# Optimization experiments

Measured on AMD Instinct MI355X. Metric: run time of the kernel, lower is better.

Reference implementation:

```python
import jax, jax.numpy as jnp
import numpy as np

SHIFTS = 1
WINDOW_SIZES = (4, 8, 16)
BN_EPS = 1e-5


def _calc_attn_path(x, ws, shifts):
    # x: (b, H, W, 2c) with channels laid out as (qv=2, c)
    b, H, W, c2 = x.shape
    c = c2 // 2
    if shifts > 0:
        x = jnp.roll(x, shift=(-ws // 2, -ws // 2), axis=(1, 2))
    h, w = H // ws, W // ws
    # 'b (h dh) (w dw) (qv c) -> qv (b h w) (dh dw c)'
    qv = x.reshape(b, h, ws, w, ws, 2, c).transpose(5, 0, 1, 3, 2, 4, 6)
    qv = qv.reshape(2, b * h * w, ws * ws * c)
    q, v = qv[0], qv[1]                       # (N, D), N = b*h*w windows, D = ws*ws*c
    atn = jax.nn.softmax(q @ q.T, axis=-1)    # (N, N) attention across windows (as in source)
    y = atn @ v                               # (N, D)
    # '(b h w) (dh dw c) -> b (h dh) (w dw) c'
    y = y.reshape(b, h, w, ws, ws, c).transpose(0, 1, 3, 2, 4, 5).reshape(b, H, W, c)
    if shifts > 0:
        y = jnp.roll(y, shift=(ws // 2, ws // 2), axis=(1, 2))
    return y, atn


def setup_inputs() -> dict:
    key = jax.random.key(0)
    ks = jax.random.split(key, 3)
    B, H, W, C = 4, 128, 128, 180
    inputs = jax.random.normal(ks[0], (B, H, W, C), jnp.float32)
    conv1_w = jax.random.normal(ks[1], (1, 1, C, 2 * C), jnp.float32) * 0.05
    conv1_b = jnp.zeros((2 * C,), jnp.float32)
    bn_scale = jnp.ones((2 * C,), jnp.float32)
    bn_bias = jnp.zeros((2 * C,), jnp.float32)
    conv2_w = jax.random.normal(ks[2], (1, 1, C, C), jnp.float32) * 0.05
    conv2_b = jnp.zeros((C,), jnp.float32)
    return {"inputs": inputs, "conv1_w": conv1_w, "conv1_b": conv1_b,
            "bn_scale": bn_scale, "bn_bias": bn_bias,
            "conv2_w": conv2_w, "conv2_b": conv2_b}


def reference(inputs, conv1_w, conv1_b, bn_scale, bn_bias, conv2_w, conv2_b):
    # 1x1 conv to 2*C channels (calc_attn=True)
    x = jnp.einsum('bhwc,cd->bhwd', inputs, conv1_w[0, 0]) + conv1_b
    # BatchNorm in training mode (batch statistics)
    mean = x.mean(axis=(0, 1, 2))
    var = x.var(axis=(0, 1, 2))
    x = (x - mean) * jax.lax.rsqrt(var + BN_EPS) * bn_scale + bn_bias
    xs = jnp.split(x, 3, axis=-1)             # three groups of 2*C/3 channels
    ys, attns = [], []
    for ws, xi in zip(WINDOW_SIZES, xs):
        y, a = _calc_attn_path(xi, ws, SHIFTS)
        ys.append(y)
        attns.append(a)
    y = jnp.concatenate(ys, axis=-1)          # back to C channels
    y = jnp.einsum('bhwc,cd->bhwd', y, conv2_w[0, 0]) + conv2_b
    return (y, *attns)
```

## Files before the change

kernel.cpp:

```cpp
#include <hip/hip_runtime.h>

typedef unsigned short u16;
typedef __bf16 bf16x8 __attribute__((ext_vector_type(8)));
typedef float f32x4 __attribute__((ext_vector_type(4)));
typedef u16 u16x4 __attribute__((ext_vector_type(4)));
typedef u16 u16x8 __attribute__((ext_vector_type(8)));

__device__ __forceinline__ u16 f2bf(float v) {
    unsigned u = __float_as_uint(v);
    unsigned r = (u + 0x7fffu + ((u >> 16) & 1u)) >> 16;
    return (u16)r;
}
__device__ __forceinline__ float bf2f(u16 u) { return __uint_as_float(((unsigned)u) << 16); }

__device__ __forceinline__ void async_cp16(const u16* g, u16* l) {
    __builtin_amdgcn_global_load_lds((const __attribute__((address_space(1))) unsigned int*)g,
                                     (__attribute__((address_space(3))) unsigned int*)l, 16, 0, 0);
}

__device__ __forceinline__ int xcd_swz(int local, int n) {
    const int q = n >> 3, r = n & 7;
    const int xcd = local & 7, j = local >> 3;
    const int base = xcd < r ? xcd * (q + 1) : r * (q + 1) + (xcd - r) * q;
    return base + j;
}

#define LKSWZ(tid) ((((tid) & 3) ^ (((tid) >> 3) & 3)) << 3)
#define ROSWZ(lane) (((lane) & 15) * 32 + ((((lane) >> 4) ^ (((lane) >> 1) & 3)) << 3))

__global__ __launch_bounds__(256) void gemm_f32(
    const u16* __restrict__ A, const u16* __restrict__ B,
    float* __restrict__ C, const float* __restrict__ bias,
    int K, int ldc, int n_store)
{
    __shared__ char smem[32768];
    u16* As = (u16*)smem;
    u16* Bs = (u16*)(smem + 8192);
    const int tid = threadIdx.x;
    const int lane = tid & 63;
    const int wave = tid >> 6;
    const int wm = wave >> 1, wn = wave & 1;
    const long m0 = (long)blockIdx.y * 128;
    const long n0 = (long)blockIdx.x * 128;

    f32x4 acc[4][4] = {};
    const int lrow = tid >> 2;
    const int lk = LKSWZ(tid);
    const u16* Ag = A + (m0 + lrow) * (long)K + lk;
    const u16* Bg = B + (n0 + lrow) * (long)K + lk;
    u16* Asl = As + tid * 8;
    u16* Bsl = Bs + tid * 8;
    const long K64 = (long)64 * K;
    const int ro = ROSWZ(lane);
    const int nsteps = K >> 5;

    async_cp16(Ag, Asl);
    async_cp16(Ag + K64, Asl + 2048);
    async_cp16(Bg, Bsl);
    async_cp16(Bg + K64, Bsl + 2048);
    __syncthreads();

    int cur = 0;
    for (int s = 0; s < nsteps; s++) {
        if (s + 1 < nsteps) {
            const int kn = (s + 1) << 5;
            u16* An = Asl + ((cur ^ 1) << 13);
            u16* Bn = Bsl + ((cur ^ 1) << 13);
            async_cp16(Ag + kn, An);
            async_cp16(Ag + kn + K64, An + 2048);
            async_cp16(Bg + kn, Bn);
            async_cp16(Bg + kn + K64, Bn + 2048);
        }
        bf16x8 af[4], bg[4];
        const u16* Asc = As + (cur << 13);
        const u16* Bsc = Bs + (cur << 13);
#pragma unroll
        for (int i = 0; i < 4; i++) af[i] = *(const bf16x8*)(Asc + (wm * 64 + i * 16) * 32 + ro);
#pragma unroll
        for (int j = 0; j < 4; j++) bg[j] = *(const bf16x8*)(Bsc + (wn * 64 + j * 16) * 32 + ro);
#pragma unroll
        for (int i = 0; i < 4; i++)
#pragma unroll
            for (int j = 0; j < 4; j++)
                acc[i][j] = __builtin_amdgcn_mfma_f32_16x16x32_bf16(af[i], bg[j], acc[i][j], 0, 0, 0);
        __syncthreads();
        cur ^= 1;
    }

    float bv[4];
#pragma unroll
    for (int j = 0; j < 4; j++) bv[j] = bias[n0 + wn * 64 + j * 16 + (lane & 15)];

    float* Cs = (float*)smem;
    for (int c = 0; c < 4; c++) {
        __syncthreads();
        if (wm == (c >> 1)) {
#pragma unroll
            for (int ii = 0; ii < 2; ii++) {
                const int i = (c & 1) * 2 + ii;
#pragma unroll
                for (int j = 0; j < 4; j++)
#pragma unroll
                    for (int r = 0; r < 4; r++) {
                        const int lr = ii * 16 + ((lane >> 4) << 2) + r;
                        Cs[lr * 128 + wn * 64 + j * 16 + (lane & 15)] = acc[i][j][r] + bv[j];
                    }
            }
        }
        __syncthreads();
        const int lr = tid >> 3;
        const int cg = (tid & 7) * 16;
        const long rowg = m0 + c * 32 + lr;
#pragma unroll
        for (int e = 0; e < 4; e++) {
            const int colg = cg + e * 4;
            if ((int)n0 + colg < n_store)
                *(f32x4*)(C + rowg * (long)ldc + n0 + colg) = *(const f32x4*)(Cs + lr * 128 + colg);
        }
    }
}

__global__ __launch_bounds__(256) void conv1_gemm(
    const float* __restrict__ A, const u16* __restrict__ B,
    u16* __restrict__ C, const float* __restrict__ bias, float* __restrict__ accum)
{
    __shared__ char smem[16384];
    u16* As = (u16*)smem;
    u16* Bs = (u16*)(smem + 8192);
    const int tid = threadIdx.x;
    const int lane = tid & 63;
    const int wave = tid >> 6;
    const int wm = wave >> 1, wn = wave & 1;
    const long m0 = (long)blockIdx.y * 128;
    const long n0 = (long)blockIdx.x * 128;

    f32x4 acc[4][4] = {};
    const int lrow = tid >> 2;
    const int lk = LKSWZ(tid);
    const float* Ar0 = A + (m0 + lrow) * 180L;
    const float* Ar1 = Ar0 + 64 * 180L;
    const u16* Bg = B + (n0 + lrow) * 192L + lk;
    u16* Asl = As + tid * 8;
    u16* Bsl = Bs + tid * 8;
    const int ro = ROSWZ(lane);

#pragma unroll
    for (int k0 = 0; k0 < 192; k0 += 32) {
        const int gk = k0 + lk;
        u16x8 oa, ob;
        if (gk + 8 <= 180) {
            f32x4 a0 = *(const f32x4*)(Ar0 + gk), a1 = *(const f32x4*)(Ar0 + gk + 4);
            f32x4 b0 = *(const f32x4*)(Ar1 + gk), b1 = *(const f32x4*)(Ar1 + gk + 4);
#pragma unroll
            for (int c = 0; c < 4; c++) {
                oa[c] = f2bf(a0[c]); oa[4 + c] = f2bf(a1[c]);
                ob[c] = f2bf(b0[c]); ob[4 + c] = f2bf(b1[c]);
            }
        } else if (gk < 180) {
            f32x4 a0 = *(const f32x4*)(Ar0 + gk);
            f32x4 b0 = *(const f32x4*)(Ar1 + gk);
#pragma unroll
            for (int c = 0; c < 4; c++) {
                oa[c] = f2bf(a0[c]); oa[4 + c] = 0;
                ob[c] = f2bf(b0[c]); ob[4 + c] = 0;
            }
        } else {
#pragma unroll
            for (int c = 0; c < 8; c++) { oa[c] = 0; ob[c] = 0; }
        }
        *(u16x8*)Asl = oa;
        *(u16x8*)(Asl + 2048) = ob;
        async_cp16(Bg + k0, Bsl);
        async_cp16(Bg + k0 + 64 * 192, Bsl + 2048);
        __syncthreads();
        bf16x8 af[4], bg[4];
#pragma unroll
        for (int i = 0; i < 4; i++) af[i] = *(const bf16x8*)(As + (wm * 64 + i * 16) * 32 + ro);
#pragma unroll
        for (int j = 0; j < 4; j++) bg[j] = *(const bf16x8*)(Bs + (wn * 64 + j * 16) * 32 + ro);
#pragma unroll
        for (int i = 0; i < 4; i++)
#pragma unroll
            for (int j = 0; j < 4; j++)
                acc[i][j] = __builtin_amdgcn_mfma_f32_16x16x32_bf16(af[i], bg[j], acc[i][j], 0, 0, 0);
        __syncthreads();
    }

    float bv[4];
#pragma unroll
    for (int j = 0; j < 4; j++) bv[j] = bias[n0 + wn * 64 + j * 16 + (lane & 15)];

    {
        float bs[4], bs2[4];
#pragma unroll
        for (int j = 0; j < 4; j++) {
            float s = 0.0f, s2 = 0.0f;
#pragma unroll
            for (int i = 0; i < 4; i++)
#pragma unroll
                for (int r = 0; r < 4; r++) {
                    const float v = bf2f(f2bf(acc[i][j][r] + bv[j]));
                    s += v; s2 += v * v;
                }
            s += __shfl_xor(s, 16, 64);  s += __shfl_xor(s, 32, 64);
            s2 += __shfl_xor(s2, 16, 64); s2 += __shfl_xor(s2, 32, 64);
            bs[j] = s; bs2[j] = s2;
        }
        if (lane < 16) {
#pragma unroll
            for (int j = 0; j < 4; j++) {
                const int ch = (int)n0 + wn * 64 + j * 16 + lane;
                atomicAdd(&accum[ch], bs[j]);
                atomicAdd(&accum[384 + ch], bs2[j]);
            }
        }
    }

    u16* Cs = (u16*)smem;
    for (int c = 0; c < 2; c++) {
        __syncthreads();
        if (wm == c) {
#pragma unroll
            for (int i = 0; i < 4; i++)
#pragma unroll
                for (int j = 0; j < 4; j++)
#pragma unroll
                    for (int r = 0; r < 4; r++) {
                        const int lr = i * 16 + ((lane >> 4) << 2) + r;
                        Cs[lr * 128 + wn * 64 + j * 16 + (lane & 15)] = f2bf(acc[i][j][r] + bv[j]);
                    }
        }
        __syncthreads();
        const int lr = tid >> 2;
        const int cg = (tid & 3) * 32;
        const long rowg = m0 + c * 64 + lr;
#pragma unroll
        for (int e = 0; e < 4; e++) {
            const int colg = cg + e * 8;
            *(u16x8*)(C + rowg * 384L + n0 + colg) = *(const u16x8*)(Cs + lr * 128 + colg);
        }
    }
}

__global__ __launch_bounds__(256) void qq_all(
    const u16* __restrict__ q0, const u16* __restrict__ q1, const u16* __restrict__ q2,
    float* __restrict__ S0, float* __restrict__ pG1, float* __restrict__ pG2)
{
    __shared__ char smem[32768];
    u16* As = (u16*)smem;
    u16* Bs = (u16*)(smem + 8192);
    const int bid = blockIdx.x;
    int seg, local;
    if (bid < 528) { seg = 0; local = xcd_swz(bid, 528); }
    else if (bid < 816) { seg = 1; local = xcd_swz(bid - 528, 288); }
    else { seg = 2; local = xcd_swz(bid - 816, 180); }
    const int tX = seg == 0 ? 32 : (seg == 1 ? 8 : 2);
    const int TT = (tX * (tX + 1)) >> 1;
    const int K = seg == 0 ? 1024 : (seg == 1 ? 3840 : 15360);
    const int Ksplit = seg == 0 ? 1024 : (seg == 1 ? 480 : 256);
    const int N = seg == 0 ? 4096 : (seg == 1 ? 1024 : 256);
    const u16* A = seg == 0 ? q0 : (seg == 1 ? q1 : q2);
    float* outP = seg == 0 ? S0 : (seg == 1 ? pG1 : pG2);
    const int z = local / TT;
    int rem = local - z * TT;
    int by = 0, rowlen = tX;
    while (rem >= rowlen) { rem -= rowlen; by++; rowlen--; }
    const int bx = by + rem;

    const int tid = threadIdx.x;
    const int lane = tid & 63;
    const int wave = tid >> 6;
    const int wm = wave >> 1, wn = wave & 1;
    const long m0 = (long)by * 128;
    const long n0 = (long)bx * 128;
    const int kbeg = z * Ksplit;

    f32x4 acc[4][4] = {};
    const int lrow = tid >> 2;
    const int lk = LKSWZ(tid);
    const u16* Ag = A + (m0 + lrow) * (long)K + lk;
    const u16* Bg = A + (n0 + lrow) * (long)K + lk;
    u16* Asl = As + tid * 8;
    u16* Bsl = Bs + tid * 8;
    const long K64 = (long)64 * K;
    const int ro = ROSWZ(lane);
    const int nsteps = Ksplit >> 5;

    async_cp16(Ag + kbeg, Asl);
    async_cp16(Ag + kbeg + K64, Asl + 2048);
    async_cp16(Bg + kbeg, Bsl);
    async_cp16(Bg + kbeg + K64, Bsl + 2048);
    __syncthreads();

    int cur = 0;
    for (int s = 0; s < nsteps; s++) {
        if (s + 1 < nsteps) {
            const int kn = kbeg + ((s + 1) << 5);
            u16* An = Asl + ((cur ^ 1) << 13);
            u16* Bn = Bsl + ((cur ^ 1) << 13);
            async_cp16(Ag + kn, An);
            async_cp16(Ag + kn + K64, An + 2048);
            async_cp16(Bg + kn, Bn);
            async_cp16(Bg + kn + K64, Bn + 2048);
        }
        bf16x8 af[4], bg[4];
        const u16* Asc = As + (cur << 13);
        const u16* Bsc = Bs + (cur << 13);
#pragma unroll
        for (int i = 0; i < 4; i++) af[i] = *(const bf16x8*)(Asc + (wm * 64 + i * 16) * 32 + ro);
#pragma unroll
        for (int j = 0; j < 4; j++) bg[j] = *(const bf16x8*)(Bsc + (wn * 64 + j * 16) * 32 + ro);
#pragma unroll
        for (int i = 0; i < 4; i++)
#pragma unroll
            for (int j = 0; j < 4; j++)
                acc[i][j] = __builtin_amdgcn_mfma_f32_16x16x32_bf16(af[i], bg[j], acc[i][j], 0, 0, 0);
        __syncthreads();
        cur ^= 1;
    }

    float* Pz = outP + (long)z * N * N;

    if (bx != by) {
        const int r0 = (int)n0 + wn * 64 + (lane & 15);
        const int c0 = (int)m0 + wm * 64 + ((lane >> 4) << 2);
#pragma unroll
        for (int j = 0; j < 4; j++) {
            float* rp = Pz + (long)(r0 + j * 16) * N + c0;
#pragma unroll
            for (int i = 0; i < 4; i++)
                *(f32x4*)(rp + i * 16) = acc[i][j];
        }
    }

    float* Cs = (float*)smem;
    for (int c = 0; c < 4; c++) {
        __syncthreads();
        if (wm == (c >> 1)) {
#pragma unroll
            for (int ii = 0; ii < 2; ii++) {
                const int i = (c & 1) * 2 + ii;
#pragma unroll
                for (int j = 0; j < 4; j++)
#pragma unroll
                    for (int r = 0; r < 4; r++) {
                        const int lr = ii * 16 + ((lane >> 4) << 2) + r;
                        Cs[lr * 128 + wn * 64 + j * 16 + (lane & 15)] = acc[i][j][r];
                    }
            }
        }
        __syncthreads();
        const int lr = tid >> 3;
        const int cg = (tid & 7) * 16;
        const long rowg = m0 + c * 32 + lr;
#pragma unroll
        for (int e = 0; e < 4; e++) {
            const int colg = cg + e * 4;
            *(f32x4*)(Pz + rowg * (long)N + n0 + colg) = *(const f32x4*)(Cs + lr * 128 + colg);
        }
    }
}

__global__ __launch_bounds__(256, 4) void pv_all(
    const u16* __restrict__ a0, const u16* __restrict__ a1, const u16* __restrict__ a2,
    const u16* __restrict__ vt0, const u16* __restrict__ vt1, const u16* __restrict__ vt2,
    u16* __restrict__ Ysp, float* __restrict__ pP0, float* __restrict__ pP1)
{
    __shared__ char smem[32768];
    u16* As = (u16*)smem;
    u16* Bs = (u16*)(smem + 8192);
    const int bid = blockIdx.x;
    int seg, local, z = 0;
    if (bid < 512) { seg = 0; const int l = xcd_swz(bid, 512); z = l >> 8; local = l & 255; }
    else if (bid < 752) { seg = 1; local = xcd_swz(bid - 512, 240); }
    else { seg = 2; local = xcd_swz(bid - 752, 240); }
    const int tX = seg == 0 ? 8 : (seg == 1 ? 30 : 120);
    const int K = seg == 0 ? 4096 : (seg == 1 ? 1024 : 256);
    const int Ksplit = seg == 0 ? 2048 : K;
    const int D = seg == 0 ? 960 : (seg == 1 ? 3840 : 15360);
    const int l2ws = 2 + seg;
    const int l2wc = 5 - seg;
    const u16* A = seg == 0 ? a0 : (seg == 1 ? a1 : a2);
    const u16* B = seg == 0 ? vt0 : (seg == 1 ? vt1 : vt2);
    const int bx = local % tX;
    const int by = local / tX;

    const int tid = threadIdx.x;
    const int lane = tid & 63;
    const int wave = tid >> 6;
    const int wm = wave >> 1, wn = wave & 1;
    const long m0 = (long)by * 128;
    const long n0 = (long)bx * 128;
    const int kbeg = z * Ksplit;

    f32x4 acc[4][4] = {};
    const int lrow = tid >> 2;
    const int lk = LKSWZ(tid);
    const u16* Ag = A + (m0 + lrow) * (long)K + lk;
    const u16* Bg = B + (n0 + lrow) * (long)K + lk;
    u16* Asl = As + tid * 8;
    u16* Bsl = Bs + tid * 8;
    const long K64 = (long)64 * K;
    const int ro = ROSWZ(lane);
    const int nsteps = Ksplit >> 5;

    async_cp16(Ag + kbeg, Asl);
    async_cp16(Ag + kbeg + K64, Asl + 2048);
    async_cp16(Bg + kbeg, Bsl);
    async_cp16(Bg + kbeg + K64, Bsl + 2048);
    __syncthreads();

    int cur = 0;
    for (int s = 0; s < nsteps; s++) {
        if (s + 1 < nsteps) {
            const int kn = kbeg + ((s + 1) << 5);
            u16* An = Asl + ((cur ^ 1) << 13);
            u16* Bn = Bsl + ((cur ^ 1) << 13);
            async_cp16(Ag + kn, An);
            async_cp16(Ag + kn + K64, An + 2048);
            async_cp16(Bg + kn, Bn);
            async_cp16(Bg + kn + K64, Bn + 2048);
        }
        bf16x8 af[4], bg[4];
        const u16* Asc = As + (cur << 13);
        const u16* Bsc = Bs + (cur << 13);
#pragma unroll
        for (int i = 0; i < 4; i++) af[i] = *(const bf16x8*)(Asc + (wm * 64 + i * 16) * 32 + ro);
#pragma unroll
        for (int j = 0; j < 4; j++) bg[j] = *(const bf16x8*)(Bsc + (wn * 64 + j * 16) * 32 + ro);
#pragma unroll
        for (int i = 0; i < 4; i++)
#pragma unroll
            for (int j = 0; j < 4; j++)
                acc[i][j] = __builtin_amdgcn_mfma_f32_16x16x32_bf16(af[i], bg[j], acc[i][j], 0, 0, 0);
        __syncthreads();
        cur ^= 1;
    }

    if (seg == 0) {
        float* Pz = (z == 0) ? pP0 : pP1;
        float* Cs = (float*)smem;
        for (int c = 0; c < 4; c++) {
            __syncthreads();
            if (wm == (c >> 1)) {
#pragma unroll
                for (int ii = 0; ii < 2; ii++) {
                    const int i = (c & 1) * 2 + ii;
#pragma unroll
                    for (int j = 0; j < 4; j++)
#pragma unroll
                        for (int r = 0; r < 4; r++) {
                            const int lr = ii * 16 + ((lane >> 4) << 2) + r;
                            Cs[lr * 128 + wn * 64 + j * 16 + (lane & 15)] = acc[i][j][r];
                        }
                }
            }
            __syncthreads();
            const int lr = tid >> 3;
            const int cg = (tid & 7) * 16;
            const long rowg = m0 + c * 32 + lr;
#pragma unroll
            for (int e = 0; e < 4; e++) {
                const int colg = cg + e * 4;
                *(f32x4*)(Pz + rowg * 1024L + n0 + colg) = *(const f32x4*)(Cs + lr * 128 + colg);
            }
        }
        return;
    }

    u16* Cs = (u16*)smem;
    const int wcm = (1 << l2wc) - 1;
    const int wsm = (1 << l2ws) - 1;
    const int sh = 1 << (l2ws - 1);
    for (int c = 0; c < 2; c++) {
        __syncthreads();
        if (wm == c) {
#pragma unroll
            for (int i = 0; i < 4; i++)
#pragma unroll
                for (int j = 0; j < 4; j++)
#pragma unroll
                    for (int r = 0; r < 4; r++) {
                        const int lr = i * 16 + ((lane >> 4) << 2) + r;
                        Cs[lr * 128 + wn * 64 + j * 16 + (lane & 15)] = f2bf(acc[i][j][r]);
                    }
        }
        __syncthreads();
        const int lr = tid >> 2;
        const int cgbase = (tid & 3) * 32;
        const int n = (int)m0 + c * 64 + lr;
        const int wi = n & wcm;
        const int hi = (n >> l2wc) & wcm;
        const int bb = n >> (2 * l2wc);
        const int rowb = (hi << l2ws) + sh;
        const int colb = (wi << l2ws) + sh;
        const long bbase = (long)bb * 128 * 128 * 192 + 60 * seg;
#pragma unroll
        for (int e = 0; e < 8; e++) {
            const int colg = cgbase + e * 4;
            const int d = (int)n0 + colg;
            if (d < D) {
                const int cc = d % 60;
                const int pp = d / 60;
                const int dh = pp >> l2ws;
                const int dw = pp & wsm;
                const int row = (rowb + dh) & 127;
                const int col = (colb + dw) & 127;
                *(u16x4*)(Ysp + bbase + ((long)row * 128 + col) * 192 + cc) =
                    *(const u16x4*)(Cs + lr * 128 + colg);
            }
        }
    }
}

__global__ __launch_bounds__(256) void reduce_scatter_g0(
    const float* __restrict__ pP0, const float* __restrict__ pP1, u16* __restrict__ Ysp)
{
    const int n = blockIdx.x;
    const int d = threadIdx.x * 4;
    if (d >= 960) return;
    const long i = (long)n * 1024 + d;
    f32x4 s = *(const f32x4*)(pP0 + i) + *(const f32x4*)(pP1 + i);
    const int cc = d % 60;
    const int pp = d / 60;
    const int dh = pp >> 2;
    const int dw = pp & 3;
    const int wi = n & 31;
    const int hi = (n >> 5) & 31;
    const int b = n >> 10;
    const int row = ((hi << 2) + dh + 2) & 127;
    const int col = ((wi << 2) + dw + 2) & 127;
    u16x4 o;
#pragma unroll
    for (int c = 0; c < 4; c++) o[c] = f2bf(s[c]);
    *(u16x4*)(Ysp + ((long)((b << 7) + row) * 128 + col) * 192 + cc) = o;
}

__global__ __launch_bounds__(192) void prep_all(
    const float* __restrict__ W1, const float* __restrict__ W2,
    const float* __restrict__ b1, const float* __restrict__ b2,
    u16* __restrict__ W1t, u16* __restrict__ W2t,
    float* __restrict__ b1p, float* __restrict__ b2p, float* __restrict__ accum)
{
    const int bid = blockIdx.x;
    const int t = threadIdx.x;
    if (bid < 384) {
        W1t[bid * 192 + t] = (bid < 360 && t < 180) ? f2bf(W1[t * 360 + bid]) : (u16)0;
    } else if (bid < 640) {
        const int n = bid - 384;
        W2t[n * 192 + t] = (n < 180 && t < 180) ? f2bf(W2[t * 180 + n]) : (u16)0;
    } else {
#pragma unroll
        for (int j = 0; j < 4; j++) {
            const int i = t + 192 * j;
            if (i < 384) b1p[i] = (i < 360) ? b1[i] : 0.0f;
            else if (i < 640) { const int k = i - 384; b2p[k] = (k < 180) ? b2[k] : 0.0f; }
            if (i < 768) accum[i] = 0.0f;
        }
    }
}

__global__ __launch_bounds__(256) void gather_all(
    const u16* __restrict__ x, const float* __restrict__ accum,
    const float* __restrict__ bns, const float* __restrict__ bnb,
    u16* __restrict__ q0, u16* __restrict__ q1, u16* __restrict__ q2,
    u16* __restrict__ vt0, u16* __restrict__ vt1, u16* __restrict__ vt2)
{
    __shared__ u16 t[64][65];
    const int bid = blockIdx.x;
    int seg, local;
    if (bid < 1024) { seg = 0; local = bid; }
    else if (bid < 1984) { seg = 1; local = bid - 1024; }
    else { seg = 2; local = bid - 1984; }
    const int tX = seg == 0 ? 16 : (seg == 1 ? 60 : 240);
    const int N = seg == 0 ? 4096 : (seg == 1 ? 1024 : 256);
    const int D = seg == 0 ? 960 : (seg == 1 ? 3840 : 15360);
    const int Dp = seg == 0 ? 1024 : (seg == 1 ? 3840 : 15360);
    const int l2ws = 2 + seg;
    const int l2wc = 5 - seg;
    u16* q = seg == 0 ? q0 : (seg == 1 ? q1 : q2);
    u16* vt = seg == 0 ? vt0 : (seg == 1 ? vt1 : vt2);
    const int bx = local % tX;
    const int by = local / tX;

    const int d0 = bx * 64;
    const int n0 = by * 64;
    const int tc = threadIdx.x & 63;
    const int tr = threadIdx.x >> 6;

    const int d = d0 + tc;
    const int sh = 1 << (l2ws - 1);
    const int cc = d % 60;
    const int pp = d / 60;
    const int dh = pp >> l2ws;
    const int dw = pp & ((1 << l2ws) - 1);
    const int wcm = (1 << l2wc) - 1;
    const int ch = 120 * seg + cc;
    const float m_q = accum[ch] * (1.0f / 65536.0f);
    const float v_q = accum[384 + ch] * (1.0f / 65536.0f) - m_q * m_q;
    const float seq = bns[ch] * rsqrtf(v_q + 1e-5f);
    const float beq = bnb[ch] - m_q * seq;
    const float m_v = accum[ch + 60] * (1.0f / 65536.0f);
    const float v_v = accum[384 + ch + 60] * (1.0f / 65536.0f) - m_v * m_v;
    const float sev = bns[ch + 60] * rsqrtf(v_v + 1e-5f);
    const float bev = bnb[ch + 60] - m_v * sev;
    const bool valid = d < D;

#pragma unroll 4
    for (int i = 0; i < 16; i++) {
        const int n = n0 + i * 4 + tr;
        const int wi = n & wcm;
        const int hi = (n >> l2wc) & wcm;
        const int b = n >> (2 * l2wc);
        const int row = ((hi << l2ws) + dh + sh) & 127;
        const int col = ((wi << l2ws) + dw + sh) & 127;
        const long src = ((long)((b << 7) + row) * 128 + col) * 384 + ch;
        const float xq = bf2f(x[src]);
        const float xv = bf2f(x[src + 60]);
        q[(long)n * Dp + d] = valid ? f2bf(seq * xq + beq) : (u16)0;
        t[tc][i * 4 + tr] = f2bf(sev * xv + bev);
    }
    __syncthreads();
#pragma unroll 4
    for (int i = 0; i < 16; i++) {
        const int dd = i * 4 + tr;
        vt[(long)(d0 + dd) * N + n0 + tc] = t[dd][tc];
    }
}

template <int VPT>
__device__ __forceinline__ void softmax_body(
    const float* __restrict__ P, int nsplit, long MN, int rowi,
    float* __restrict__ S, u16* __restrict__ Sb)
{
    const int N = VPT * 256;
    const long base = (long)rowi * N;
    float v[VPT];
    float mx = -3.0e38f;
#pragma unroll
    for (int i = 0; i < VPT; i++) {
        const long idx = base + i * 256 + threadIdx.x;
        float val = P[idx];
        for (int z = 1; z < nsplit; z++) val += P[(long)z * MN + idx];
        v[i] = val; mx = fmaxf(mx, val);
    }
#pragma unroll
    for (int o = 32; o > 0; o >>= 1) mx = fmaxf(mx, __shfl_down(mx, o, 64));
    __shared__ float redm[4];
    if ((threadIdx.x & 63) == 0) redm[threadIdx.x >> 6] = mx;
    __syncthreads();
    mx = fmaxf(fmaxf(redm[0], redm[1]), fmaxf(redm[2], redm[3]));
    float s = 0.0f;
#pragma unroll
    for (int i = 0; i < VPT; i++) { v[i] = __expf(v[i] - mx); s += v[i]; }
#pragma unroll
    for (int o = 32; o > 0; o >>= 1) s += __shfl_down(s, o, 64);
    __shared__ float reds[4];
    if ((threadIdx.x & 63) == 0) reds[threadIdx.x >> 6] = s;
    __syncthreads();
    s = reds[0] + reds[1] + reds[2] + reds[3];
    const float inv = 1.0f / s;
#pragma unroll
    for (int i = 0; i < VPT; i++) {
        const float r = v[i] * inv;
        const long idx = base + i * 256 + threadIdx.x;
        S[idx] = r;
        Sb[idx] = f2bf(r);
    }
}

__global__ __launch_bounds__(256) void softmax_all(
    float* __restrict__ S0, const float* __restrict__ pG1, const float* __restrict__ pG2,
    float* __restrict__ out1, float* __restrict__ out2,
    u16* __restrict__ ab0, u16* __restrict__ ab1, u16* __restrict__ ab2,
    u16* __restrict__ Ysp)
{
    const int r = blockIdx.x;
    if (r >= 5376) {
        const long rr = (long)(r - 5376) * 256 + threadIdx.x;
        u16* p = Ysp + rr * 192 + 180;
        const u16x4 zz = {0, 0, 0, 0};
        *(u16x4*)(p) = zz;
        *(u16x4*)(p + 4) = zz;
        *(u16x4*)(p + 8) = zz;
        return;
    }
    if (r < 4096)      softmax_body<16>(S0, 1, 16777216L, r, S0, ab0);
    else if (r < 5120) softmax_body<4>(pG1, 8, 1048576L, r - 4096, out1, ab1);
    else               softmax_body<1>(pG2, 60, 65536L, r - 5120, out2, ab2);
}

extern "C" void kernel_launch(void* const* d_in, const int* in_sizes, int n_in,
                              void* d_out, int out_size, void* d_ws, size_t ws_size,
                              hipStream_t stream)
{
    const float* in_x = (const float*)d_in[0];
    const float* w1  = (const float*)d_in[1];
    const float* b1  = (const float*)d_in[2];
    const float* bns = (const float*)d_in[3];
    const float* bnb = (const float*)d_in[4];
    const float* w2  = (const float*)d_in[5];
    const float* b2  = (const float*)d_in[6];
    float* out = (float*)d_out;

    char* w = (char*)d_ws;
    u16* atnb0 = (u16*)w;
    size_t off = 33554432;
    u16* x = (u16*)(w + off);
    float* pG1 = (float*)(w + off);
    float* pG2 = (float*)(w + off + 33554432);
    u16* Ysp = (u16*)(w + off);
    float* pP1 = (float*)(w + off + 25165824);
    off += 50331648;
    u16* W1t = (u16*)(w + off);  off += 147456;
    u16* W2t = (u16*)(w + off);  off += 98304;
    float* b1p = (float*)(w + off);   off += 4096;
    float* b2p = (float*)(w + off);   off += 4096;
    float* accum = (float*)(w + off); off += 4096;
    u16* q0 = (u16*)(w + off);  off += 8388608;
    u16* q1 = (u16*)(w + off);  off += 7864320;
    u16* q2 = (u16*)(w + off);  off += 7864320;
    u16* vt0 = (u16*)(w + off); off += 8388608;
    u16* vt1 = (u16*)(w + off); off += 7864320;
    u16* vt2 = (u16*)(w + off); off += 7864320;
    u16* atnb1 = (u16*)(w + off); off += 2097152;
    u16* atnb2 = (u16*)(w + off); off += 131072;
    float* pP0 = (float*)q0;

    float* S0 = out + 11796480L;
    float* S1 = out + 28573696L;
    float* S2 = out + 29622272L;

    prep_all<<<641, 192, 0, stream>>>(w1, w2, b1, b2, W1t, W2t, b1p, b2p, accum);
    conv1_gemm<<<dim3(3, 512), 256, 0, stream>>>(in_x, W1t, x, b1p, accum);
    gather_all<<<2944, 256, 0, stream>>>(x, accum, bns, bnb, q0, q1, q2, vt0, vt1, vt2);
    qq_all<<<996, 256, 0, stream>>>(q0, q1, q2, S0, pG1, pG2);
    softmax_all<<<5632, 256, 0, stream>>>(S0, pG1, pG2, S1, S2, atnb0, atnb1, atnb2, Ysp);
    pv_all<<<992, 256, 0, stream>>>(atnb0, atnb1, atnb2, vt0, vt1, vt2, Ysp, pP0, pP1);
    reduce_scatter_g0<<<4096, 256, 0, stream>>>(pP0, pP1, Ysp);
    gemm_f32<<<dim3(2, 512), 256, 0, stream>>>(Ysp, W2t, out, b2p, 192, 180, 180);
}
```

Before: 418.7 us.

## Pre-convert conv1 input to padded bf16 and double-buffer conv1 GEMM loads

Measured after the change: 413.6 us. About the same (-1.2%).

```diff
diff --git a/kernel.cpp b/kernel.cpp
--- a/kernel.cpp
+++ b/kernel.cpp
@@ -27,6 +27,21 @@
 
 #define LKSWZ(tid) ((((tid) & 3) ^ (((tid) >> 3) & 3)) << 3)
 #define ROSWZ(lane) (((lane) & 15) * 32 + ((((lane) >> 4) ^ (((lane) >> 1) & 3)) << 3))
+
+__global__ __launch_bounds__(256) void conv_a_bf16(
+    const float* __restrict__ A, u16* __restrict__ Abf)
+{
+    const long idx = (long)blockIdx.x * 256 + threadIdx.x;
+    const long row = idx / 48;
+    const int q = (int)(idx - row * 48);
+    u16x4 o = {0, 0, 0, 0};
+    if (q < 45) {
+        const f32x4 v = *(const f32x4*)(A + row * 180L + q * 4);
+#pragma unroll
+        for (int c = 0; c < 4; c++) o[c] = f2bf(v[c]);
+    }
+    *(u16x4*)(Abf + row * 192L + q * 4) = o;
+}
 
 __global__ __launch_bounds__(256) void gemm_f32(
     const u16* __restrict__ A, const u16* __restrict__ B,
@@ -121,10 +136,10 @@
 }
 
 __global__ __launch_bounds__(256) void conv1_gemm(
-    const float* __restrict__ A, const u16* __restrict__ B,
+    const u16* __restrict__ A, const u16* __restrict__ B,
     u16* __restrict__ C, const float* __restrict__ bias, float* __restrict__ accum)
 {
-    __shared__ char smem[16384];
+    __shared__ char smem[32768];
     u16* As = (u16*)smem;
     u16* Bs = (u16*)(smem + 8192);
     const int tid = threadIdx.x;
@@ -137,53 +152,45 @@
     f32x4 acc[4][4] = {};
     const int lrow = tid >> 2;
     const int lk = LKSWZ(tid);
-    const float* Ar0 = A + (m0 + lrow) * 180L;
-    const float* Ar1 = Ar0 + 64 * 180L;
+    const u16* Ag = A + (m0 + lrow) * 192L + lk;
     const u16* Bg = B + (n0 + lrow) * 192L + lk;
     u16* Asl = As + tid * 8;
     u16* Bsl = Bs + tid * 8;
+    const long K64 = 64L * 192;
     const int ro = ROSWZ(lane);
-
-#pragma unroll
-    for (int k0 = 0; k0 < 192; k0 += 32) {
-        const int gk = k0 + lk;
-        u16x8 oa, ob;
-        if (gk + 8 <= 180) {
-            f32x4 a0 = *(const f32x4*)(Ar0 + gk), a1 = *(const f32x4*)(Ar0 + gk + 4);
-            f32x4 b0 = *(const f32x4*)(Ar1 + gk), b1 = *(const f32x4*)(Ar1 + gk + 4);
-#pragma unroll
-            for (int c = 0; c < 4; c++) {
-                oa[c] = f2bf(a0[c]); oa[4 + c] = f2bf(a1[c]);
-                ob[c] = f2bf(b0[c]); ob[4 + c] = f2bf(b1[c]);
-            }
-        } else if (gk < 180) {
-            f32x4 a0 = *(const f32x4*)(Ar0 + gk);
-            f32x4 b0 = *(const f32x4*)(Ar1 + gk);
-#pragma unroll
-            for (int c = 0; c < 4; c++) {
-                oa[c] = f2bf(a0[c]); oa[4 + c] = 0;
-                ob[c] = f2bf(b0[c]); ob[4 + c] = 0;
-            }
-        } else {
-#pragma unroll
-            for (int c = 0; c < 8; c++) { oa[c] = 0; ob[c] = 0; }
-        }
-        *(u16x8*)Asl = oa;
-        *(u16x8*)(Asl + 2048) = ob;
-        async_cp16(Bg + k0, Bsl);
-        async_cp16(Bg + k0 + 64 * 192, Bsl + 2048);
-        __syncthreads();
+    const int nsteps = 6;
+
+    async_cp16(Ag, Asl);
+    async_cp16(Ag + K64, Asl + 2048);
+    async_cp16(Bg, Bsl);
+    async_cp16(Bg + K64, Bsl + 2048);
+    __syncthreads();
+
+    int cur = 0;
+    for (int s = 0; s < nsteps; s++) {
+        if (s + 1 < nsteps) {
+            const int kn = (s + 1) << 5;
+            u16* An = Asl + ((cur ^ 1) << 13);
+            u16* Bn = Bsl + ((cur ^ 1) << 13);
+            async_cp16(Ag + kn, An);
+            async_cp16(Ag + kn + K64, An + 2048);
+            async_cp16(Bg + kn, Bn);
+            async_cp16(Bg + kn + K64, Bn + 2048);
+        }
         bf16x8 af[4], bg[4];
-#pragma unroll
-        for (int i = 0; i < 4; i++) af[i] = *(const bf16x8*)(As + (wm * 64 + i * 16) * 32 + ro);
-#pragma unroll
-        for (int j = 0; j < 4; j++) bg[j] = *(const bf16x8*)(Bs + (wn * 64 + j * 16) * 32 + ro);
+        const u16* Asc = As + (cur << 13);
+        const u16* Bsc = Bs + (cur << 13);
+#pragma unroll
+        for (int i = 0; i < 4; i++) af[i] = *(const bf16x8*)(Asc + (wm * 64 + i * 16) * 32 + ro);
+#pragma unroll
+        for (int j = 0; j < 4; j++) bg[j] = *(const bf16x8*)(Bsc + (wn * 64 + j * 16) * 32 + ro);
 #pragma unroll
         for (int i = 0; i < 4; i++)
 #pragma unroll
             for (int j = 0; j < 4; j++)
                 acc[i][j] = __builtin_amdgcn_mfma_f32_16x16x32_bf16(af[i], bg[j], acc[i][j], 0, 0, 0);
         __syncthreads();
+        cur ^= 1;
     }
 
     float bv[4];
@@ -726,13 +733,15 @@
     u16* atnb1 = (u16*)(w + off); off += 2097152;
     u16* atnb2 = (u16*)(w + off); off += 131072;
     float* pP0 = (float*)q0;
+    u16* Abf = q0;
 
     float* S0 = out + 11796480L;
     float* S1 = out + 28573696L;
     float* S2 = out + 29622272L;
 
     prep_all<<<641, 192, 0, stream>>>(w1, w2, b1, b2, W1t, W2t, b1p, b2p, accum);
-    conv1_gemm<<<dim3(3, 512), 256, 0, stream>>>(in_x, W1t, x, b1p, accum);
+    conv_a_bf16<<<12288, 256, 0, stream>>>(in_x, Abf);
+    conv1_gemm<<<dim3(3, 512), 256, 0, stream>>>(Abf, W1t, x, b1p, accum);
     gather_all<<<2944, 256, 0, stream>>>(x, accum, bns, bnb, q0, q1, q2, vt0, vt1, vt2);
     qq_all<<<996, 256, 0, stream>>>(q0, q1, q2, S0, pG1, pG2);
     softmax_all<<<5632, 256, 0, stream>>>(S0, pG1, pG2, S1, S2, atnb0, atnb1, atnb2, Ysp);
```
